# Performance work log

Hardware: AMD Instinct MI355X
Metric: run time of the kernel (lower is better)

The kernel has to match this reference:

```python
import jax, jax.numpy as jnp
import numpy as np

D = 768          # hidden_size
M = 8            # num_patchmerges
B = 16
S = 2048         # non-CLF tokens


def setup_inputs() -> dict:
    key = jax.random.key(0)
    ks = jax.random.split(key, 12)
    std = 0.02
    tokens = jax.random.normal(ks[0], (B, 1 + S, D), dtype=jnp.float32)
    lengths = jnp.maximum(jax.random.randint(ks[1], (B,), 0, S), 1).astype(jnp.int64)
    # PatchMerger: learned queries + layernorm params
    q = jax.random.normal(ks[2], (M, D), dtype=jnp.float32) * std
    ln_scale = jnp.ones((D,), dtype=jnp.float32)
    ln_bias = jnp.zeros((D,), dtype=jnp.float32)
    # mlp1: Linear(3D, D) -> GELU -> Linear(D, D)
    w1a = jax.random.normal(ks[3], (3 * D, D), dtype=jnp.float32) * std
    b1a = jnp.zeros((D,), dtype=jnp.float32)
    w2a = jax.random.normal(ks[4], (D, D), dtype=jnp.float32) * std
    b2a = jnp.zeros((D,), dtype=jnp.float32)
    # mlp2: Linear((1+M)D, D) -> GELU -> Linear(D, D)
    w1b = jax.random.normal(ks[5], ((1 + M) * D, D), dtype=jnp.float32) * std
    b1b = jnp.zeros((D,), dtype=jnp.float32)
    w2b = jax.random.normal(ks[6], (D, D), dtype=jnp.float32) * std
    b2b = jnp.zeros((D,), dtype=jnp.float32)
    return dict(tokens=tokens, lengths=lengths, q=q, ln_scale=ln_scale,
                ln_bias=ln_bias, w1a=w1a, b1a=b1a, w2a=w2a, b2a=b2a,
                w1b=w1b, b1b=b1b, w2b=w2b, b2b=b2b)


def _hpmlp(x, w1, b1, w2, b2):
    h = jax.nn.gelu(x @ w1 + b1, approximate=False)  # dropout=0 -> identity
    return h @ w2 + b2


def _layernorm(x, scale, bias, eps=1e-5):
    mu = jnp.mean(x, axis=-1, keepdims=True)
    var = jnp.var(x, axis=-1, keepdims=True)
    return (x - mu) * jax.lax.rsqrt(var + eps) * scale + bias


def reference(tokens, lengths, q, ln_scale, ln_bias,
              w1a, b1a, w2a, b2a, w1b, b1b, w2b, b2b):
    clf = tokens[:, 0]            # [B, D]
    x = tokens[:, 1:]             # [B, S, D]
    mask = jnp.arange(S)[None, :] < lengths[:, None]   # [B, S]
    mf = mask[..., None].astype(x.dtype)

    # fixed path: masked mean / max / min over valid tokens
    denom = lengths.astype(x.dtype)[:, None]
    mean_p = jnp.sum(x * mf, axis=1) / denom
    max_p = jnp.max(jnp.where(mask[..., None], x, -jnp.inf), axis=1)
    min_p = jnp.min(jnp.where(mask[..., None], x, jnp.inf), axis=1)
    pooled_trad = jnp.concatenate([mean_p, max_p, min_p], axis=-1)  # [B, 3D]
    out_fixed = _hpmlp(pooled_trad, w1a, b1a, w2a, b2a)

    # learned path: PatchMerger (masked attention from M learned queries)
    xn = _layernorm(x, ln_scale, ln_bias)
    scores = jnp.einsum('md,bsd->bms', q, xn) / jnp.sqrt(jnp.asarray(D, x.dtype))
    scores = jnp.where(mask[:, None, :], scores, -jnp.inf)
    attn = jax.nn.softmax(scores, axis=-1)                # [B, M, S]
    merged = jnp.einsum('bms,bsd->bmd', attn, x)          # [B, M, D]
    pooled_learn = jnp.concatenate([merged.reshape(B, M * D), clf], axis=-1)
    out_learn = _hpmlp(pooled_learn, w1b, b1b, w2b, b2b)

    return jnp.concatenate([out_fixed, out_learn], axis=-1)  # [B, 2D]
```

## Files before the change

kernel.cpp:

```cpp
#include <hip/hip_runtime.h>
#include <math.h>

#define SD 768
#define SB 16
#define SM 8
#define SS 2048
#define TOK_ROW 2049
#define NEG_INF (-__builtin_inff())

#define OFF_PPOOL   0
#define OFF_PO      1179648
#define OFF_PML     4325376
#define OFF_PTRAD   4333568
#define OFF_PLEARN  4370432
#define OFF_P1A     4481024
#define OFF_P1B     4702208
#define OFF_HA      5365760
#define OFF_HB      5378048
#define OFF_P2A     5390336
#define OFF_P2B     5464064

__device__ __forceinline__ int clen(int v) { return v < 1 ? 1 : (v > SS ? SS : v); }

__global__ __launch_bounds__(256, 2) void k1_flash(
    const float* __restrict__ tokens, const int* __restrict__ lengths,
    const float* __restrict__ q, const float* __restrict__ lns,
    const float* __restrict__ lnb, float* __restrict__ ppool,
    float* __restrict__ pO, float* __restrict__ pml) {
  int c = blockIdx.x, b = blockIdx.y;
  int len = clen(lengths[b]);
  int c0 = c * 64;
  if (c0 >= len) return;
  int tid = threadIdx.x, w = tid >> 6, lane = tid & 63;
  int mm = lane & 7;

  __shared__ float p_lds[4][16][8];
  __shared__ float pool_lds[4][3][SD];
  __shared__ float O_lds[SM][SD];
  __shared__ float mx_lds[8];

  {
    float* pf = &p_lds[0][0][0];
    for (int i = tid; i < 512; i += 256) pf[i] = NEG_INF;
  }

  float4 qr[8][3];
  float qs1sel, qbsel;
  {
    float4 l4[3], lb4[3];
    #pragma unroll
    for (int g = 0; g < 3; ++g) {
      l4[g] = *(const float4*)(lns + g * 256 + lane * 4);
      lb4[g] = *(const float4*)(lnb + g * 256 + lane * 4);
    }
    float qs1r[8], qbr[8];
    #pragma unroll
    for (int m = 0; m < 8; ++m) {
      float s1 = 0.f, sb = 0.f;
      #pragma unroll
      for (int g = 0; g < 3; ++g) {
        float4 qv = *(const float4*)(q + m * SD + g * 256 + lane * 4);
        float4 qs;
        qs.x = qv.x * l4[g].x; qs.y = qv.y * l4[g].y;
        qs.z = qv.z * l4[g].z; qs.w = qv.w * l4[g].w;
        qr[m][g] = qs;
        s1 += qs.x + qs.y + qs.z + qs.w;
        sb += qv.x * lb4[g].x + qv.y * lb4[g].y + qv.z * lb4[g].z + qv.w * lb4[g].w;
      }
      #pragma unroll
      for (int o = 32; o; o >>= 1) { s1 += __shfl_xor(s1, o, 64); sb += __shfl_xor(sb, o, 64); }
      qs1r[m] = s1; qbr[m] = sb;
    }
    qs1sel = qs1r[0]; qbsel = qbr[0];
    #pragma unroll
    for (int m = 1; m < 8; ++m) {
      qs1sel = (mm == m) ? qs1r[m] : qs1sel;
      qbsel = (mm == m) ? qbr[m] : qbsel;
    }
  }
  __syncthreads();

  float psum[12], pmax[12], pmin[12];
  #pragma unroll
  for (int j = 0; j < 12; ++j) { psum[j] = 0.f; pmax[j] = NEG_INF; pmin[j] = -NEG_INF; }

  int srow = c0 + w * 16;
  int smax = len - srow; if (smax > 16) smax = 16; if (smax < 0) smax = 0;
  const float* xrow = tokens + ((size_t)b * TOK_ROW + 1 + srow) * SD;

  float4 nx0 = {}, nx1 = {}, nx2 = {};
  if (smax > 0) {
    nx0 = *(const float4*)(xrow + lane * 4);
    nx1 = *(const float4*)(xrow + 256 + lane * 4);
    nx2 = *(const float4*)(xrow + 512 + lane * 4);
  }
  for (int i = 0; i < smax; ++i) {
    float4 x0 = nx0, x1 = nx1, x2 = nx2;
    if (i + 1 < smax) {
      const float* xq = xrow + (size_t)(i + 1) * SD;
      nx0 = *(const float4*)(xq + lane * 4);
      nx1 = *(const float4*)(xq + 256 + lane * 4);
      nx2 = *(const float4*)(xq + 512 + lane * 4);
    }
    float xv[12] = {x0.x, x0.y, x0.z, x0.w, x1.x, x1.y, x1.z, x1.w,
                    x2.x, x2.y, x2.z, x2.w};
    float s1 = 0.f, s2 = 0.f;
    #pragma unroll
    for (int j = 0; j < 12; ++j) {
      float v = xv[j];
      psum[j] += v;
      pmax[j] = fmaxf(pmax[j], v);
      pmin[j] = fminf(pmin[j], v);
      s1 += v;
      s2 += v * v;
    }
    float d[8];
    #pragma unroll
    for (int m = 0; m < 8; ++m) {
      float4 a0 = qr[m][0], a1 = qr[m][1], a2 = qr[m][2];
      d[m] = a0.x * xv[0] + a0.y * xv[1] + a0.z * xv[2] + a0.w * xv[3]
           + a1.x * xv[4] + a1.y * xv[5] + a1.z * xv[6] + a1.w * xv[7]
           + a2.x * xv[8] + a2.y * xv[9] + a2.z * xv[10] + a2.w * xv[11];
    }
    #pragma unroll
    for (int o = 1; o <= 4; o <<= 1)
      #pragma unroll
      for (int m = 0; m < 8; ++m) d[m] += __shfl_xor(d[m], o, 64);
    float u = d[0];
    #pragma unroll
    for (int m = 1; m < 8; ++m) u = (mm == m) ? d[m] : u;
    #pragma unroll
    for (int o = 8; o <= 32; o <<= 1) {
      u += __shfl_xor(u, o, 64);
      s1 += __shfl_xor(s1, o, 64);
      s2 += __shfl_xor(s2, o, 64);
    }
    #pragma unroll
    for (int o = 1; o <= 4; o <<= 1) { s1 += __shfl_xor(s1, o, 64); s2 += __shfl_xor(s2, o, 64); }
    float mu = s1 * (1.f / 768.f);
    float var = s2 * (1.f / 768.f) - mu * mu;
    float rstd = rsqrtf(var + 1e-5f);
    float sc = (rstd * u - rstd * mu * qs1sel + qbsel) * 0.03608439182435161f;
    if (lane < 8) p_lds[w][i][lane] = sc;
  }

  #pragma unroll
  for (int g = 0; g < 3; ++g) {
    int dd = g * 256 + lane * 4;
    *(float4*)&pool_lds[w][0][dd] = make_float4(psum[g*4], psum[g*4+1], psum[g*4+2], psum[g*4+3]);
    *(float4*)&pool_lds[w][1][dd] = make_float4(pmax[g*4], pmax[g*4+1], pmax[g*4+2], pmax[g*4+3]);
    *(float4*)&pool_lds[w][2][dd] = make_float4(pmin[g*4], pmin[g*4+1], pmin[g*4+2], pmin[g*4+3]);
  }
  __syncthreads();

  float* pf = &p_lds[0][0][0];
  if (tid < 8) {
    float mxv = NEG_INF;
    for (int r = 0; r < 64; ++r) mxv = fmaxf(mxv, pf[r * 8 + tid]);
    mx_lds[tid] = mxv;
  }
  __syncthreads();
  for (int e = tid; e < 512; e += 256) {
    int m = e & 7;
    pf[e] = __expf(pf[e] - mx_lds[m]);
  }
  __syncthreads();
  if (tid < 8) {
    float lv = 0.f;
    for (int r = 0; r < 64; ++r) lv += pf[r * 8 + tid];
    size_t base = (size_t)(c * SB + b) * 16;
    pml[base + tid] = mx_lds[tid];
    pml[base + 8 + tid] = lv;
  }

  float O[8][12];
  #pragma unroll
  for (int m = 0; m < 8; ++m)
    #pragma unroll
    for (int j = 0; j < 12; ++j) O[m][j] = 0.f;
  float4 a0v = {}, a1v = {}, a2v = {}, b0v = {}, b1v = {}, b2v = {};
  if (smax > 0) {
    a0v = *(const float4*)(xrow + lane * 4);
    a1v = *(const float4*)(xrow + 256 + lane * 4);
    a2v = *(const float4*)(xrow + 512 + lane * 4);
  }
  if (smax > 1) {
    const float* xq = xrow + SD;
    b0v = *(const float4*)(xq + lane * 4);
    b1v = *(const float4*)(xq + 256 + lane * 4);
    b2v = *(const float4*)(xq + 512 + lane * 4);
  }
  for (int i = 0; i < smax; ++i) {
    float4 x0 = a0v, x1 = a1v, x2 = a2v;
    a0v = b0v; a1v = b1v; a2v = b2v;
    if (i + 2 < smax) {
      const float* xq = xrow + (size_t)(i + 2) * SD;
      b0v = *(const float4*)(xq + lane * 4);
      b1v = *(const float4*)(xq + 256 + lane * 4);
      b2v = *(const float4*)(xq + 512 + lane * 4);
    }
    float xv[12] = {x0.x, x0.y, x0.z, x0.w, x1.x, x1.y, x1.z, x1.w,
                    x2.x, x2.y, x2.z, x2.w};
    const float4* pr = (const float4*)&p_lds[w][i][0];
    float4 pa = pr[0], pb = pr[1];
    float pm[8] = {pa.x, pa.y, pa.z, pa.w, pb.x, pb.y, pb.z, pb.w};
    #pragma unroll
    for (int m = 0; m < 8; ++m)
      #pragma unroll
      for (int j = 0; j < 12; ++j) O[m][j] += pm[m] * xv[j];
  }
  #pragma unroll
  for (int r = 0; r < 4; ++r) {
    if (w == r) {
      #pragma unroll
      for (int m = 0; m < 8; ++m)
        #pragma unroll
        for (int g = 0; g < 3; ++g) {
          int dd = g * 256 + lane * 4;
          float4 mine = make_float4(O[m][g*4], O[m][g*4+1], O[m][g*4+2], O[m][g*4+3]);
          if (r == 0) {
            *(float4*)&O_lds[m][dd] = mine;
          } else {
            float4 cur = *(float4*)&O_lds[m][dd];
            cur.x += mine.x; cur.y += mine.y; cur.z += mine.z; cur.w += mine.w;
            *(float4*)&O_lds[m][dd] = cur;
          }
        }
    }
    __syncthreads();
  }

  size_t obase = (size_t)(c * SB + b) * 6144;
  const float* of = &O_lds[0][0];
  for (int j = tid * 4; j < 6144; j += 1024)
    *(float4*)&pO[obase + j] = *(const float4*)&of[j];

  size_t pbase = (size_t)(c * SB + b) * 2304;
  for (int j4 = tid * 4; j4 < 2304; j4 += 1024) {
    int stat = j4 / SD, dd = j4 - stat * SD;
    float4 v0 = *(float4*)&pool_lds[0][stat][dd];
    float4 v1 = *(float4*)&pool_lds[1][stat][dd];
    float4 v2 = *(float4*)&pool_lds[2][stat][dd];
    float4 v3 = *(float4*)&pool_lds[3][stat][dd];
    float4 r;
    if (stat == 0) {
      r.x = v0.x + v1.x + v2.x + v3.x; r.y = v0.y + v1.y + v2.y + v3.y;
      r.z = v0.z + v1.z + v2.z + v3.z; r.w = v0.w + v1.w + v2.w + v3.w;
    } else if (stat == 1) {
      r.x = fmaxf(fmaxf(v0.x, v1.x), fmaxf(v2.x, v3.x));
      r.y = fmaxf(fmaxf(v0.y, v1.y), fmaxf(v2.y, v3.y));
      r.z = fmaxf(fmaxf(v0.z, v1.z), fmaxf(v2.z, v3.z));
      r.w = fmaxf(fmaxf(v0.w, v1.w), fmaxf(v2.w, v3.w));
    } else {
      r.x = fminf(fminf(v0.x, v1.x), fminf(v2.x, v3.x));
      r.y = fminf(fminf(v0.y, v1.y), fminf(v2.y, v3.y));
      r.z = fminf(fminf(v0.z, v1.z), fminf(v2.z, v3.z));
      r.w = fminf(fminf(v0.w, v1.w), fminf(v2.w, v3.w));
    }
    *(float4*)&ppool[pbase + j4] = r;
  }
}

__global__ void k_combine(const float* __restrict__ ppool, const float* __restrict__ pO,
                          const float* __restrict__ pml, const float* __restrict__ tokens,
                          const int* __restrict__ lengths,
                          float* __restrict__ ptrad, float* __restrict__ plearn) {
  int tile = blockIdx.x, b = blockIdx.y;
  int len = clen(lengths[b]);
  int nv = (len + 63) >> 6;
  int tid = threadIdx.x;
  __shared__ float pml_lds[32][16];
  __shared__ float e_lds[32][8];
  __shared__ float Linv_lds[8];
  for (int t = tid; t < nv * 16; t += 256) {
    int cc = t >> 4, j = t & 15;
    pml_lds[cc][j] = pml[(size_t)(cc * SB + b) * 16 + j];
  }
  __syncthreads();
  if (tid < 8) {
    float M = NEG_INF;
    for (int cc = 0; cc < nv; ++cc) M = fmaxf(M, pml_lds[cc][tid]);
    float L = 0.f;
    for (int cc = 0; cc < nv; ++cc) {
      float e = __expf(pml_lds[cc][tid] - M);
      e_lds[cc][tid] = e;
      L += e * pml_lds[cc][8 + tid];
    }
    Linv_lds[tid] = 1.f / L;
  }
  __syncthreads();
  #pragma unroll
  for (int k = 0; k < 4; ++k) {
    int jj = tile * 1024 + k * 256 + tid;
    if (jj < 2304) {
      int stat = jj / SD;
      const float* pp = ppool + jj + (size_t)b * 2304;
      if (stat == 0) {
        float a0 = 0.f, a1 = 0.f, a2 = 0.f, a3 = 0.f;
        int cc = 0;
        for (; cc + 4 <= nv; cc += 4) {
          a0 += pp[(size_t)(cc    ) * SB * 2304];
          a1 += pp[(size_t)(cc + 1) * SB * 2304];
          a2 += pp[(size_t)(cc + 2) * SB * 2304];
          a3 += pp[(size_t)(cc + 3) * SB * 2304];
        }
        for (; cc < nv; ++cc) a0 += pp[(size_t)cc * SB * 2304];
        ptrad[b * 2304 + jj] = ((a0 + a1) + (a2 + a3)) / (float)len;
      } else if (stat == 1) {
        float a0 = NEG_INF, a1 = NEG_INF, a2 = NEG_INF, a3 = NEG_INF;
        int cc = 0;
        for (; cc + 4 <= nv; cc += 4) {
          a0 = fmaxf(a0, pp[(size_t)(cc    ) * SB * 2304]);
          a1 = fmaxf(a1, pp[(size_t)(cc + 1) * SB * 2304]);
          a2 = fmaxf(a2, pp[(size_t)(cc + 2) * SB * 2304]);
          a3 = fmaxf(a3, pp[(size_t)(cc + 3) * SB * 2304]);
        }
        for (; cc < nv; ++cc) a0 = fmaxf(a0, pp[(size_t)cc * SB * 2304]);
        ptrad[b * 2304 + jj] = fmaxf(fmaxf(a0, a1), fmaxf(a2, a3));
      } else {
        float a0 = -NEG_INF, a1 = -NEG_INF, a2 = -NEG_INF, a3 = -NEG_INF;
        int cc = 0;
        for (; cc + 4 <= nv; cc += 4) {
          a0 = fminf(a0, pp[(size_t)(cc    ) * SB * 2304]);
          a1 = fminf(a1, pp[(size_t)(cc + 1) * SB * 2304]);
          a2 = fminf(a2, pp[(size_t)(cc + 2) * SB * 2304]);
          a3 = fminf(a3, pp[(size_t)(cc + 3) * SB * 2304]);
        }
        for (; cc < nv; ++cc) a0 = fminf(a0, pp[(size_t)cc * SB * 2304]);
        ptrad[b * 2304 + jj] = fminf(fminf(a0, a1), fminf(a2, a3));
      }
    } else if (jj < 8448) {
      int t = jj - 2304;
      int m = t / SD;
      const float* po = pO + t + (size_t)b * 6144;
      float a0 = 0.f, a1 = 0.f, a2 = 0.f, a3 = 0.f;
      float a4 = 0.f, a5 = 0.f, a6 = 0.f, a7 = 0.f;
      int cc = 0;
      for (; cc + 8 <= nv; cc += 8) {
        a0 += po[(size_t)(cc    ) * SB * 6144] * e_lds[cc    ][m];
        a1 += po[(size_t)(cc + 1) * SB * 6144] * e_lds[cc + 1][m];
        a2 += po[(size_t)(cc + 2) * SB * 6144] * e_lds[cc + 2][m];
        a3 += po[(size_t)(cc + 3) * SB * 6144] * e_lds[cc + 3][m];
        a4 += po[(size_t)(cc + 4) * SB * 6144] * e_lds[cc + 4][m];
        a5 += po[(size_t)(cc + 5) * SB * 6144] * e_lds[cc + 5][m];
        a6 += po[(size_t)(cc + 6) * SB * 6144] * e_lds[cc + 6][m];
        a7 += po[(size_t)(cc + 7) * SB * 6144] * e_lds[cc + 7][m];
      }
      for (; cc < nv; ++cc) a0 += po[(size_t)cc * SB * 6144] * e_lds[cc][m];
      plearn[b * 6912 + t] = (((a0 + a1) + (a2 + a3)) + ((a4 + a5) + (a6 + a7))) * Linv_lds[m];
    } else {
      int dd = jj - 8448;
      plearn[b * 6912 + 6144 + dd] = tokens[(size_t)b * TOK_ROW * SD + dd];
    }
  }
}

__global__ __launch_bounds__(256) void gemm_partial(
    const float* __restrict__ XA, const float* __restrict__ WA, int ktA, float* __restrict__ PA,
    const float* __restrict__ XB, const float* __restrict__ WB, float* __restrict__ PB) {
  int nt = blockIdx.x, ky = blockIdx.y;
  const float *X, *W; float* P; int kt, ktN;
  if (ky < ktA) { X = XA; W = WA; P = PA; kt = ky; ktN = ktA; }
  else { X = XB; W = WB; P = PB; kt = ky - ktA; ktN = gridDim.y - ktA; }
  int K = ktN * 128;
  int k0 = kt * 128;
  __shared__ __align__(16) float xt[128 * 20];
  __shared__ float red[4][64][17];
  int tid = threadIdx.x;
  int kk = tid & 127, half = tid >> 7;
  #pragma unroll
  for (int u = 0; u < 8; ++u) {
    int b2 = half * 8 + u;
    xt[kk * 20 + b2] = X[b2 * K + k0 + kk];
  }
  __syncthreads();
  int w = tid >> 6, lane = tid & 63;
  int n = nt * 64 + lane;
  float acc[16];
  #pragma unroll
  for (int b2 = 0; b2 < 16; ++b2) acc[b2] = 0.f;
  const float* Wp = W + (size_t)k0 * SD + n;
  #pragma unroll 8
  for (int kj = 0; kj < 32; ++kj) {
    int k = w + kj * 4;
    float wv = Wp[(size_t)k * SD];
    const float4* xr = reinterpret_cast<const float4*>(xt + k * 20);
    float4 a0 = xr[0], a1 = xr[1], a2 = xr[2], a3 = xr[3];
    acc[0] += wv * a0.x; acc[1] += wv * a0.y; acc[2] += wv * a0.z; acc[3] += wv * a0.w;
    acc[4] += wv * a1.x; acc[5] += wv * a1.y; acc[6] += wv * a1.z; acc[7] += wv * a1.w;
    acc[8] += wv * a2.x; acc[9] += wv * a2.y; acc[10] += wv * a2.z; acc[11] += wv * a2.w;
    acc[12] += wv * a3.x; acc[13] += wv * a3.y; acc[14] += wv * a3.z; acc[15] += wv * a3.w;
  }
  #pragma unroll
  for (int b2 = 0; b2 < 16; ++b2) red[w][lane][b2] = acc[b2];
  __syncthreads();
  for (int i = tid; i < 1024; i += 256) {
    int nn = i & 63, b2 = i >> 6;
    float r = red[0][nn][b2] + red[1][nn][b2] + red[2][nn][b2] + red[3][nn][b2];
    P[(size_t)(kt * 16 + b2) * SD + nt * 64 + nn] = r;
  }
}

__global__ void gelu_reduce(const float* __restrict__ PA, const float* __restrict__ b1a,
                            float* __restrict__ HA, const float* __restrict__ PB,
                            const float* __restrict__ b1b, float* __restrict__ HB) {
  int y = blockIdx.y;
  int j = blockIdx.x * 256 + threadIdx.x;
  float r;
  if (y == 0) {
    r = b1a[j % SD];
    #pragma unroll
    for (int kt = 0; kt < 18; ++kt) r += PA[kt * 12288 + j];
    HA[j] = r * 0.5f * (1.f + erff(r * 0.70710678118654752f));
  } else {
    r = b1b[j % SD];
    #pragma unroll
    for (int kt = 0; kt < 54; ++kt) r += PB[kt * 12288 + j];
    HB[j] = r * 0.5f * (1.f + erff(r * 0.70710678118654752f));
  }
}

__global__ void final_reduce(const float* __restrict__ P2A, const float* __restrict__ b2a,
                             const float* __restrict__ P2B, const float* __restrict__ b2b,
                             float* __restrict__ out) {
  int y = blockIdx.y;
  const float* P = y ? P2B : P2A;
  const float* bias = y ? b2b : b2a;
  int j = blockIdx.x * 256 + threadIdx.x;
  float r = bias[j % SD];
  #pragma unroll
  for (int kt = 0; kt < 6; ++kt) r += P[kt * 12288 + j];
  int b = j / SD, nn = j - b * SD;
  out[b * 1536 + y * SD + nn] = r;
}

extern "C" void kernel_launch(void* const* d_in, const int* in_sizes, int n_in,
                              void* d_out, int out_size, void* d_ws, size_t ws_size,
                              hipStream_t stream) {
  const float* tokens = (const float*)d_in[0];
  const int* lengths  = (const int*)d_in[1];
  const float* q      = (const float*)d_in[2];
  const float* lns    = (const float*)d_in[3];
  const float* lnb    = (const float*)d_in[4];
  const float* w1a    = (const float*)d_in[5];
  const float* b1a    = (const float*)d_in[6];
  const float* w2a    = (const float*)d_in[7];
  const float* b2a    = (const float*)d_in[8];
  const float* w1b    = (const float*)d_in[9];
  const float* b1b    = (const float*)d_in[10];
  const float* w2b    = (const float*)d_in[11];
  const float* b2b    = (const float*)d_in[12];
  float* ws  = (float*)d_ws;
  float* out = (float*)d_out;

  float* ppool  = ws + OFF_PPOOL;
  float* pO     = ws + OFF_PO;
  float* pml    = ws + OFF_PML;
  float* ptrad  = ws + OFF_PTRAD;
  float* plearn = ws + OFF_PLEARN;
  float* p1a    = ws + OFF_P1A;
  float* p1b    = ws + OFF_P1B;
  float* ha     = ws + OFF_HA;
  float* hb     = ws + OFF_HB;
  float* p2a    = ws + OFF_P2A;
  float* p2b    = ws + OFF_P2B;

  k1_flash<<<dim3(32, 16), 256, 0, stream>>>(tokens, lengths, q, lns, lnb, ppool, pO, pml);
  k_combine<<<dim3(9, 16), 256, 0, stream>>>(ppool, pO, pml, tokens, lengths, ptrad, plearn);
  gemm_partial<<<dim3(12, 72), 256, 0, stream>>>(ptrad, w1a, 18, p1a, plearn, w1b, p1b);
  gelu_reduce<<<dim3(48, 2), 256, 0, stream>>>(p1a, b1a, ha, p1b, b1b, hb);
  gemm_partial<<<dim3(12, 12), 256, 0, stream>>>(ha, w2a, 6, p2a, hb, w2b, p2b);
  final_reduce<<<dim3(48, 2), 256, 0, stream>>>(p2a, b2a, p2b, b2b, out);
}
```

Measured before the change: 230.6 us.

## Merge flash scoring and accumulation into one pass; fuse GELU reduce into second GEMM

The patch-merger kernel now computes layernorm scores, exponentials and the weighted sum in a single pass over each token chunk, instead of a scoring pass followed by a second read of the tokens. It drops the running-max subtraction, so the combine step only sums the per-chunk denominators and no longer rescales. The GELU partial-sum reduction is folded into the staging step of the second GEMM, which removes one kernel launch and the HA/HB round trip. The trade-offs are higher register pressure (launch bounds lowered to one block per SM) and a softmax that can overflow if the scores become large.

```diff
diff --git a/kernel.cpp b/kernel.cpp
--- a/kernel.cpp
+++ b/kernel.cpp
@@ -15,14 +15,12 @@
 #define OFF_PLEARN  4370432
 #define OFF_P1A     4481024
 #define OFF_P1B     4702208
-#define OFF_HA      5365760
-#define OFF_HB      5378048
 #define OFF_P2A     5390336
 #define OFF_P2B     5464064
 
 __device__ __forceinline__ int clen(int v) { return v < 1 ? 1 : (v > SS ? SS : v); }
 
-__global__ __launch_bounds__(256, 2) void k1_flash(
+__global__ __launch_bounds__(256, 1) void k1_flash(
     const float* __restrict__ tokens, const int* __restrict__ lengths,
     const float* __restrict__ q, const float* __restrict__ lns,
     const float* __restrict__ lnb, float* __restrict__ ppool,
@@ -34,15 +32,9 @@
   int tid = threadIdx.x, w = tid >> 6, lane = tid & 63;
   int mm = lane & 7;
 
-  __shared__ float p_lds[4][16][8];
   __shared__ float pool_lds[4][3][SD];
   __shared__ float O_lds[SM][SD];
-  __shared__ float mx_lds[8];
-
-  {
-    float* pf = &p_lds[0][0][0];
-    for (int i = tid; i < 512; i += 256) pf[i] = NEG_INF;
-  }
+  __shared__ float l_lds[4][8];
 
   float4 qr[8][3];
   float qs1sel, qbsel;
@@ -78,106 +70,21 @@
       qbsel = (mm == m) ? qbr[m] : qbsel;
     }
   }
-  __syncthreads();
 
   float psum[12], pmax[12], pmin[12];
   #pragma unroll
   for (int j = 0; j < 12; ++j) { psum[j] = 0.f; pmax[j] = NEG_INF; pmin[j] = -NEG_INF; }
+  float O[8][12];
+  #pragma unroll
+  for (int m = 0; m < 8; ++m)
+    #pragma unroll
+    for (int j = 0; j < 12; ++j) O[m][j] = 0.f;
+  float lacc = 0.f;
 
   int srow = c0 + w * 16;
   int smax = len - srow; if (smax > 16) smax = 16; if (smax < 0) smax = 0;
   const float* xrow = tokens + ((size_t)b * TOK_ROW + 1 + srow) * SD;
 
-  float4 nx0 = {}, nx1 = {}, nx2 = {};
-  if (smax > 0) {
-    nx0 = *(const float4*)(xrow + lane * 4);
-    nx1 = *(const float4*)(xrow + 256 + lane * 4);
-    nx2 = *(const float4*)(xrow + 512 + lane * 4);
-  }
-  for (int i = 0; i < smax; ++i) {
-    float4 x0 = nx0, x1 = nx1, x2 = nx2;
-    if (i + 1 < smax) {
-      const float* xq = xrow + (size_t)(i + 1) * SD;
-      nx0 = *(const float4*)(xq + lane * 4);
-      nx1 = *(const float4*)(xq + 256 + lane * 4);
-      nx2 = *(const float4*)(xq + 512 + lane * 4);
-    }
-    float xv[12] = {x0.x, x0.y, x0.z, x0.w, x1.x, x1.y, x1.z, x1.w,
-                    x2.x, x2.y, x2.z, x2.w};
-    float s1 = 0.f, s2 = 0.f;
-    #pragma unroll
-    for (int j = 0; j < 12; ++j) {
-      float v = xv[j];
-      psum[j] += v;
-      pmax[j] = fmaxf(pmax[j], v);
-      pmin[j] = fminf(pmin[j], v);
-      s1 += v;
-      s2 += v * v;
-    }
-    float d[8];
-    #pragma unroll
-    for (int m = 0; m < 8; ++m) {
-      float4 a0 = qr[m][0], a1 = qr[m][1], a2 = qr[m][2];
-      d[m] = a0.x * xv[0] + a0.y * xv[1] + a0.z * xv[2] + a0.w * xv[3]
-           + a1.x * xv[4] + a1.y * xv[5] + a1.z * xv[6] + a1.w * xv[7]
-           + a2.x * xv[8] + a2.y * xv[9] + a2.z * xv[10] + a2.w * xv[11];
-    }
-    #pragma unroll
-    for (int o = 1; o <= 4; o <<= 1)
-      #pragma unroll
-      for (int m = 0; m < 8; ++m) d[m] += __shfl_xor(d[m], o, 64);
-    float u = d[0];
-    #pragma unroll
-    for (int m = 1; m < 8; ++m) u = (mm == m) ? d[m] : u;
-    #pragma unroll
-    for (int o = 8; o <= 32; o <<= 1) {
-      u += __shfl_xor(u, o, 64);
-      s1 += __shfl_xor(s1, o, 64);
-      s2 += __shfl_xor(s2, o, 64);
-    }
-    #pragma unroll
-    for (int o = 1; o <= 4; o <<= 1) { s1 += __shfl_xor(s1, o, 64); s2 += __shfl_xor(s2, o, 64); }
-    float mu = s1 * (1.f / 768.f);
-    float var = s2 * (1.f / 768.f) - mu * mu;
-    float rstd = rsqrtf(var + 1e-5f);
-    float sc = (rstd * u - rstd * mu * qs1sel + qbsel) * 0.03608439182435161f;
-    if (lane < 8) p_lds[w][i][lane] = sc;
-  }
-
-  #pragma unroll
-  for (int g = 0; g < 3; ++g) {
-    int dd = g * 256 + lane * 4;
-    *(float4*)&pool_lds[w][0][dd] = make_float4(psum[g*4], psum[g*4+1], psum[g*4+2], psum[g*4+3]);
-    *(float4*)&pool_lds[w][1][dd] = make_float4(pmax[g*4], pmax[g*4+1], pmax[g*4+2], pmax[g*4+3]);
-    *(float4*)&pool_lds[w][2][dd] = make_float4(pmin[g*4], pmin[g*4+1], pmin[g*4+2], pmin[g*4+3]);
-  }
-  __syncthreads();
-
-  float* pf = &p_lds[0][0][0];
-  if (tid < 8) {
-    float mxv = NEG_INF;
-    for (int r = 0; r < 64; ++r) mxv = fmaxf(mxv, pf[r * 8 + tid]);
-    mx_lds[tid] = mxv;
-  }
-  __syncthreads();
-  for (int e = tid; e < 512; e += 256) {
-    int m = e & 7;
-    pf[e] = __expf(pf[e] - mx_lds[m]);
-  }
-  __syncthreads();
-  if (tid < 8) {
-    float lv = 0.f;
-    for (int r = 0; r < 64; ++r) lv += pf[r * 8 + tid];
-    size_t base = (size_t)(c * SB + b) * 16;
-    pml[base + tid] = mx_lds[tid];
-    pml[base + 8 + tid] = lv;
-  }
-
-  float O[8][12];
-  #pragma unroll
-  for (int m = 0; m < 8; ++m)
-    #pragma unroll
-    for (int j = 0; j < 12; ++j) O[m][j] = 0.f;
   float4 a0v = {}, a1v = {}, a2v = {}, b0v = {}, b1v = {}, b2v = {};
   if (smax > 0) {
     a0v = *(const float4*)(xrow + lane * 4);
@@ -201,14 +108,67 @@
     }
     float xv[12] = {x0.x, x0.y, x0.z, x0.w, x1.x, x1.y, x1.z, x1.w,
                     x2.x, x2.y, x2.z, x2.w};
-    const float4* pr = (const float4*)&p_lds[w][i][0];
-    float4 pa = pr[0], pb = pr[1];
-    float pm[8] = {pa.x, pa.y, pa.z, pa.w, pb.x, pb.y, pb.z, pb.w};
+    float s1 = 0.f, s2 = 0.f;
+    #pragma unroll
+    for (int j = 0; j < 12; ++j) {
+      float v = xv[j];
+      psum[j] += v;
+      pmax[j] = fmaxf(pmax[j], v);
+      pmin[j] = fminf(pmin[j], v);
+      s1 += v;
+      s2 += v * v;
+    }
+    float d[8];
+    #pragma unroll
+    for (int m = 0; m < 8; ++m) {
+      float4 a0 = qr[m][0], a1 = qr[m][1], a2 = qr[m][2];
+      d[m] = a0.x * xv[0] + a0.y * xv[1] + a0.z * xv[2] + a0.w * xv[3]
+           + a1.x * xv[4] + a1.y * xv[5] + a1.z * xv[6] + a1.w * xv[7]
+           + a2.x * xv[8] + a2.y * xv[9] + a2.z * xv[10] + a2.w * xv[11];
+    }
+    #pragma unroll
+    for (int o = 1; o <= 4; o <<= 1)
+      #pragma unroll
+      for (int m = 0; m < 8; ++m) d[m] += __shfl_xor(d[m], o, 64);
+    float u = d[0];
+    #pragma unroll
+    for (int m = 1; m < 8; ++m) u = (mm == m) ? d[m] : u;
+    #pragma unroll
+    for (int o = 8; o <= 32; o <<= 1) {
+      u += __shfl_xor(u, o, 64);
+      s1 += __shfl_xor(s1, o, 64);
+      s2 += __shfl_xor(s2, o, 64);
+    }
+    #pragma unroll
+    for (int o = 1; o <= 4; o <<= 1) { s1 += __shfl_xor(s1, o, 64); s2 += __shfl_xor(s2, o, 64); }
+    float mu = s1 * (1.f / 768.f);
+    float var = s2 * (1.f / 768.f) - mu * mu;
+    float rstd = rsqrtf(var + 1e-5f);
+    float sc = (rstd * u - rstd * mu * qs1sel + qbsel) * 0.03608439182435161f;
+    float p = __expf(sc);
+    lacc += p;
+    float pm[8];
+    #pragma unroll
+    for (int mi = 0; mi < 8; ++mi) pm[mi] = __shfl(p, (lane & 56) | mi, 64);
     #pragma unroll
     for (int m = 0; m < 8; ++m)
       #pragma unroll
       for (int j = 0; j < 12; ++j) O[m][j] += pm[m] * xv[j];
   }
+
+  if (lane < 8) l_lds[w][lane] = lacc;
+  #pragma unroll
+  for (int g = 0; g < 3; ++g) {
+    int dd = g * 256 + lane * 4;
+    *(float4*)&pool_lds[w][0][dd] = make_float4(psum[g*4], psum[g*4+1], psum[g*4+2], psum[g*4+3]);
+    *(float4*)&pool_lds[w][1][dd] = make_float4(pmax[g*4], pmax[g*4+1], pmax[g*4+2], pmax[g*4+3]);
+    *(float4*)&pool_lds[w][2][dd] = make_float4(pmin[g*4], pmin[g*4+1], pmin[g*4+2], pmin[g*4+3]);
+  }
+  __syncthreads();
+  if (tid < 8)
+    pml[(size_t)(c * SB + b) * 8 + tid] =
+        l_lds[0][tid] + l_lds[1][tid] + l_lds[2][tid] + l_lds[3][tid];
+
   #pragma unroll
   for (int r = 0; r < 4; ++r) {
     if (w == r) {
@@ -269,23 +229,14 @@
   int len = clen(lengths[b]);
   int nv = (len + 63) >> 6;
   int tid = threadIdx.x;
-  __shared__ float pml_lds[32][16];
-  __shared__ float e_lds[32][8];
+  __shared__ float l_sh[32][8];
   __shared__ float Linv_lds[8];
-  for (int t = tid; t < nv * 16; t += 256) {
-    int cc = t >> 4, j = t & 15;
-    pml_lds[cc][j] = pml[(size_t)(cc * SB + b) * 16 + j];
-  }
+  for (int t = tid; t < nv * 8; t += 256)
+    l_sh[t >> 3][t & 7] = pml[(size_t)((t >> 3) * SB + b) * 8 + (t & 7)];
   __syncthreads();
   if (tid < 8) {
-    float M = NEG_INF;
-    for (int cc = 0; cc < nv; ++cc) M = fmaxf(M, pml_lds[cc][tid]);
     float L = 0.f;
-    for (int cc = 0; cc < nv; ++cc) {
-      float e = __expf(pml_lds[cc][tid] - M);
-      e_lds[cc][tid] = e;
-      L += e * pml_lds[cc][8 + tid];
-    }
+    for (int cc = 0; cc < nv; ++cc) L += l_sh[cc][tid];
     Linv_lds[tid] = 1.f / L;
   }
   __syncthreads();
@@ -337,16 +288,16 @@
       float a4 = 0.f, a5 = 0.f, a6 = 0.f, a7 = 0.f;
       int cc = 0;
       for (; cc + 8 <= nv; cc += 8) {
-        a0 += po[(size_t)(cc    ) * SB * 6144] * e_lds[cc    ][m];
-        a1 += po[(size_t)(cc + 1) * SB * 6144] * e_lds[cc + 1][m];
-        a2 += po[(size_t)(cc + 2) * SB * 6144] * e_lds[cc + 2][m];
-        a3 += po[(size_t)(cc + 3) * SB * 6144] * e_lds[cc + 3][m];
-        a4 += po[(size_t)(cc + 4) * SB * 6144] * e_lds[cc + 4][m];
-        a5 += po[(size_t)(cc + 5) * SB * 6144] * e_lds[cc + 5][m];
-        a6 += po[(size_t)(cc + 6) * SB * 6144] * e_lds[cc + 6][m];
-        a7 += po[(size_t)(cc + 7) * SB * 6144] * e_lds[cc + 7][m];
+        a0 += po[(size_t)(cc    ) * SB * 6144];
+        a1 += po[(size_t)(cc + 1) * SB * 6144];
+        a2 += po[(size_t)(cc + 2) * SB * 6144];
+        a3 += po[(size_t)(cc + 3) * SB * 6144];
+        a4 += po[(size_t)(cc + 4) * SB * 6144];
+        a5 += po[(size_t)(cc + 5) * SB * 6144];
+        a6 += po[(size_t)(cc + 6) * SB * 6144];
+        a7 += po[(size_t)(cc + 7) * SB * 6144];
       }
-      for (; cc < nv; ++cc) a0 += po[(size_t)cc * SB * 6144] * e_lds[cc][m];
+      for (; cc < nv; ++cc) a0 += po[(size_t)cc * SB * 6144];
       plearn[b * 6912 + t] = (((a0 + a1) + (a2 + a3)) + ((a4 + a5) + (a6 + a7))) * Linv_lds[m];
     } else {
       int dd = jj - 8448;
@@ -401,22 +352,60 @@
   }
 }
 
-__global__ void gelu_reduce(const float* __restrict__ PA, const float* __restrict__ b1a,
-                            float* __restrict__ HA, const float* __restrict__ PB,
-                            const float* __restrict__ b1b, float* __restrict__ HB) {
-  int y = blockIdx.y;
-  int j = blockIdx.x * 256 + threadIdx.x;
-  float r;
-  if (y == 0) {
-    r = b1a[j % SD];
-    #pragma unroll
-    for (int kt = 0; kt < 18; ++kt) r += PA[kt * 12288 + j];
-    HA[j] = r * 0.5f * (1.f + erff(r * 0.70710678118654752f));
-  } else {
-    r = b1b[j % SD];
-    #pragma unroll
-    for (int kt = 0; kt < 54; ++kt) r += PB[kt * 12288 + j];
-    HB[j] = r * 0.5f * (1.f + erff(r * 0.70710678118654752f));
+template <int NP>
+__device__ __forceinline__ void stage_gelu(const float* __restrict__ P1,
+                                           const float* __restrict__ bias,
+                                           float* __restrict__ xt, int k0, int tid) {
+  int kk = tid & 127, half = tid >> 7;
+  #pragma unroll
+  for (int u = 0; u < 8; ++u) {
+    int b2 = half * 8 + u;
+    float r = bias[k0 + kk];
+    const float* p = P1 + (size_t)b2 * SD + k0 + kk;
+    #pragma unroll
+    for (int kt2 = 0; kt2 < NP; ++kt2) r += p[(size_t)kt2 * 12288];
+    xt[kk * 20 + b2] = r * 0.5f * (1.f + erff(r * 0.70710678118654752f));
+  }
+}
+
+__global__ __launch_bounds__(256) void gemm2_gelu(
+    const float* __restrict__ P1A, const float* __restrict__ b1a,
+    const float* __restrict__ W2A, float* __restrict__ P2A,
+    const float* __restrict__ P1B, const float* __restrict__ b1b,
+    const float* __restrict__ W2B, float* __restrict__ P2B) {
+  int nt = blockIdx.x, ky = blockIdx.y;
+  __shared__ __align__(16) float xt[128 * 20];
+  __shared__ float red[4][64][17];
+  int tid = threadIdx.x;
+  const float* W; float* P2; int kt;
+  if (ky < 6) { kt = ky; W = W2A; P2 = P2A; stage_gelu<18>(P1A, b1a, xt, kt * 128, tid); }
+  else { kt = ky - 6; W = W2B; P2 = P2B; stage_gelu<54>(P1B, b1b, xt, kt * 128, tid); }
+  int k0 = kt * 128;
+  __syncthreads();
+  int w = tid >> 6, lane = tid & 63;
+  int n = nt * 64 + lane;
+  float acc[16];
+  #pragma unroll
+  for (int b2 = 0; b2 < 16; ++b2) acc[b2] = 0.f;
+  const float* Wp = W + (size_t)k0 * SD + n;
+  #pragma unroll 8
+  for (int kj = 0; kj < 32; ++kj) {
+    int k = w + kj * 4;
+    float wv = Wp[(size_t)k * SD];
+    const float4* xr = reinterpret_cast<const float4*>(xt + k * 20);
+    float4 a0 = xr[0], a1 = xr[1], a2 = xr[2], a3 = xr[3];
+    acc[0] += wv * a0.x; acc[1] += wv * a0.y; acc[2] += wv * a0.z; acc[3] += wv * a0.w;
+    acc[4] += wv * a1.x; acc[5] += wv * a1.y; acc[6] += wv * a1.z; acc[7] += wv * a1.w;
+    acc[8] += wv * a2.x; acc[9] += wv * a2.y; acc[10] += wv * a2.z; acc[11] += wv * a2.w;
+    acc[12] += wv * a3.x; acc[13] += wv * a3.y; acc[14] += wv * a3.z; acc[15] += wv * a3.w;
+  }
+  #pragma unroll
+  for (int b2 = 0; b2 < 16; ++b2) red[w][lane][b2] = acc[b2];
+  __syncthreads();
+  for (int i = tid; i < 1024; i += 256) {
+    int nn = i & 63, b2 = i >> 6;
+    float r = red[0][nn][b2] + red[1][nn][b2] + red[2][nn][b2] + red[3][nn][b2];
+    P2[(size_t)(kt * 16 + b2) * SD + nt * 64 + nn] = r;
   }
 }
 
@@ -460,15 +449,12 @@
   float* plearn = ws + OFF_PLEARN;
   float* p1a    = ws + OFF_P1A;
   float* p1b    = ws + OFF_P1B;
-  float* ha     = ws + OFF_HA;
-  float* hb     = ws + OFF_HB;
   float* p2a    = ws + OFF_P2A;
   float* p2b    = ws + OFF_P2B;
 
   k1_flash<<<dim3(32, 16), 256, 0, stream>>>(tokens, lengths, q, lns, lnb, ppool, pO, pml);
   k_combine<<<dim3(9, 16), 256, 0, stream>>>(ppool, pO, pml, tokens, lengths, ptrad, plearn);
   gemm_partial<<<dim3(12, 72), 256, 0, stream>>>(ptrad, w1a, 18, p1a, plearn, w1b, p1b);
-  gelu_reduce<<<dim3(48, 2), 256, 0, stream>>>(p1a, b1a, ha, p1b, b1b, hb);
-  gemm_partial<<<dim3(12, 12), 256, 0, stream>>>(ha, w2a, 6, p2a, hb, w2b, p2b);
+  gemm2_gelu<<<dim3(12, 12), 256, 0, stream>>>(p1a, b1a, w2a, p2a, p1b, b1b, w2b, p2b);
   final_reduce<<<dim3(48, 2), 256, 0, stream>>>(p2a, b2a, p2b, b2b, out);
 }
```

Result: slower. 266.8 us (+15.7%).
